# Performance work log

Measured on AMD Instinct MI355X. Metric: run time of the kernel, lower is better.

Reference implementation:

```python
import jax, jax.numpy as jnp
import numpy as np

B, INP, OUP, FGROUP, H, W = 32, 256, 256, 8, 64, 64
CG = INP // FGROUP  # channels per group in GLGF fc1 layers


def conv3x3(x, w):
    # x: (N,1,H,W), w: (1,1,3,3); stride 1, padding 1 (SAME)
    return jax.lax.conv_general_dilated(
        x, w, window_strides=(1, 1), padding='SAME',
        dimension_numbers=('NCHW', 'OIHW', 'NCHW'))


def setup_inputs() -> dict:
    key = jax.random.key(0)
    ks = jax.random.split(key, 8)
    return {
        'x': jax.random.normal(ks[0], (B, INP, H, W), dtype=jnp.float32),
        # GLGF params (all 1x1 convs, bias=False), stored as dense matrices
        'w1l': jax.random.normal(ks[1], (FGROUP, CG, CG), dtype=jnp.float32) * 0.05,   # wn_fc1_l (groups=fgroup)
        'w1g1': jax.random.normal(ks[2], (FGROUP, CG), dtype=jnp.float32) * 0.05,      # wn_fc1_g1 (inp->fgroup, groups=fgroup)
        'w1g2': jax.random.normal(ks[3], (INP, FGROUP), dtype=jnp.float32) * 0.05,     # wn_fc1_g2 (fgroup->inp dense)
        'w2l': jax.random.normal(ks[4], (INP, OUP), dtype=jnp.float32) * 0.05,         # wn_fc2_l (groups=inp): input ch i -> oup outputs
        'w2g': jax.random.normal(ks[5], (INP,), dtype=jnp.float32) * 0.05,             # wn_fc2_g (inp->1 dense)
        'conv1_w': jax.random.normal(ks[6], (1, 1, 3, 3), dtype=jnp.float32) * 0.1,
        'conv2_w': jax.random.normal(ks[7], (1, 1, 3, 3), dtype=jnp.float32) * 0.1,
    }


def reference(x, w1l, w1g1, w1g2, w2l, w2g, conv1_w, conv2_w):
    b, c, h, w_ = x.shape
    fgroup, cg, _ = w1l.shape
    oup = w2l.shape[1]

    # adaptive_avg_pool2d(x, (1,1)) -> (B, inp) descriptor
    g = x.mean(axis=(2, 3))                                   # (B, inp)
    gg = g.reshape(b, fgroup, cg)

    # GLGF: fc1_l (grouped) + fc1_g2(fc1_g1) (squeeze to fgroup then expand)
    local = jnp.einsum('bgi,goi->bgo', gg, w1l).reshape(b, c)  # (B, inp)
    glob = jnp.einsum('bgi,gi->bg', gg, w1g1) @ w1g2.T         # (B, inp)
    s = jax.nn.sigmoid(local + glob)                           # (B, inp)

    # fc2_l (groups=inp): torch channel order is (input_ch g, out j) -> g*oup + j
    # fc2_g adds a per-sample scalar to every channel
    xw = s[:, :, None] * w2l + (s @ w2g)[:, None, None]        # (B, inp, oup)
    # WA_1Conv reinterprets the flat (oup*inp) channels as (oup, inp)
    Wdyn = xw.reshape(b, oup, c)                               # (B, oup, inp)

    # grouped conv with groups=batch, ksize=1 == per-sample matmul
    y = jnp.einsum('bihw,boi->bohw', x, Wdyn)                  # (B, oup, H, W)

    # channel gating: mean over channels -> conv3x3 -> sigmoid -> conv3x3
    cmap = y.mean(axis=1, keepdims=True)                       # (B, 1, H, W)
    cmap = conv3x3(cmap, conv1_w)
    cmap = jax.nn.sigmoid(cmap)
    cmap = conv3x3(cmap, conv2_w)
    return y * cmap
```

## Files before the change

kernel.cpp:

```cpp
#include <hip/hip_runtime.h>
#include <hip/hip_bf16.h>

typedef float  f32x4  __attribute__((ext_vector_type(4)));
typedef short  bf16x8 __attribute__((ext_vector_type(8)));

__device__ __forceinline__ short f2bf(float f) {
    union { __hip_bfloat16 h; short s; } u;
    u.h = __float2bfloat16(f);
    return u.s;
}

__device__ __forceinline__ void gload_lds16(const void* g, void* l) {
    __builtin_amdgcn_global_load_lds(
        (const __attribute__((address_space(1))) unsigned int*)g,
        (__attribute__((address_space(3))) unsigned int*)l, 16, 0, 0);
}

__global__ __launch_bounds__(256) void transpose_kernel(const float* __restrict__ x,
                                                        short* __restrict__ xt,
                                                        float* __restrict__ gpart) {
    const int pchunk = blockIdx.x;
    const int c0 = blockIdx.y * 64;
    const int b  = blockIdx.z;
    const int tid = threadIdx.x;
    const int cpair = tid >> 3;
    const int poct  = tid & 7;
    const int p0 = pchunk * 64;

    __shared__ unsigned int tile[64 * 32];

    const float* rowA = x + ((size_t)(b * 256 + c0 + 2 * cpair)) * 4096 + p0 + poct * 8;
    const float* rowB = rowA + 4096;
    float av[8], bv[8];
    *reinterpret_cast<float4*>(&av[0]) = *reinterpret_cast<const float4*>(rowA);
    *reinterpret_cast<float4*>(&av[4]) = *reinterpret_cast<const float4*>(rowA + 4);
    *reinterpret_cast<float4*>(&bv[0]) = *reinterpret_cast<const float4*>(rowB);
    *reinterpret_cast<float4*>(&bv[4]) = *reinterpret_cast<const float4*>(rowB + 4);

    float sA = 0.f, sB = 0.f;
    #pragma unroll
    for (int e = 0; e < 8; ++e) { sA += av[e]; sB += bv[e]; }
    sA += __shfl_xor(sA, 1, 64); sA += __shfl_xor(sA, 2, 64); sA += __shfl_xor(sA, 4, 64);
    sB += __shfl_xor(sB, 1, 64); sB += __shfl_xor(sB, 2, 64); sB += __shfl_xor(sB, 4, 64);
    if (poct == 0) {
        gpart[((size_t)(b * 256 + c0 + 2 * cpair)) * 64 + pchunk] = sA;
        gpart[((size_t)(b * 256 + c0 + 2 * cpair + 1)) * 64 + pchunk] = sB;
    }

    const int s = cpair >> 2, w = cpair & 3;
    #pragma unroll
    for (int e = 0; e < 8; ++e) {
        int p = poct * 8 + e;
        unsigned int u = (unsigned int)(unsigned short)f2bf(av[e]) |
                         ((unsigned int)(unsigned short)f2bf(bv[e]) << 16);
        tile[p * 32 + ((s ^ poct) << 2) + w] = u;
    }
    __syncthreads();

    const int so = tid & 7;
    #pragma unroll
    for (int h = 0; h < 2; ++h) {
        int p = (tid >> 3) + h * 32;
        int sp = so ^ ((p >> 3) & 7);
        uint4 v = *reinterpret_cast<const uint4*>(&tile[p * 32 + sp * 4]);
        *reinterpret_cast<uint4*>(xt + ((size_t)b * 4096 + p0 + p) * 256 + c0 + so * 8) = v;
    }
}

__global__ __launch_bounds__(256) void prep_kernel(
    const float* __restrict__ gpart, const float* __restrict__ w1l,
    const float* __restrict__ w1g1, const float* __restrict__ w1g2,
    const float* __restrict__ w2l, const float* __restrict__ w2g,
    float* __restrict__ s_out, float* __restrict__ t_out,
    float* __restrict__ q_out, short* __restrict__ w2l_bf) {
    int b = blockIdx.x;
    int tid = threadIdx.x;
    if (b >= 32) {
        int seg = b - 32;
        const float* src = w2l + seg * 4096;
        short* dst = w2l_bf + seg * 4096;
        #pragma unroll
        for (int it = 0; it < 4; ++it) {
            float4 v = *reinterpret_cast<const float4*>(src + it * 1024 + tid * 4);
            short4 o;
            o.x = f2bf(v.x); o.y = f2bf(v.y); o.z = f2bf(v.z); o.w = f2bf(v.w);
            *reinterpret_cast<short4*>(dst + it * 1024 + tid * 4) = o;
        }
        return;
    }
    __shared__ float gs[256];
    __shared__ float zs[8];
    __shared__ float ss[256];
    __shared__ float red[4];
    {
        const float4* gp = reinterpret_cast<const float4*>(gpart + (size_t)(b * 256 + tid) * 64);
        float acc = 0.f;
        #pragma unroll
        for (int j = 0; j < 16; ++j) { float4 v = gp[j]; acc += v.x + v.y + v.z + v.w; }
        gs[tid] = acc * (1.0f / 4096.0f);
    }
    __syncthreads();
    if (tid < 8) {
        float z = 0.f;
        for (int i = 0; i < 32; ++i) z += gs[tid * 32 + i] * w1g1[tid * 32 + i];
        zs[tid] = z;
    }
    __syncthreads();
    int grp = tid >> 5, o = tid & 31;
    float local = 0.f;
    #pragma unroll 4
    for (int i = 0; i < 32; ++i) local += gs[grp * 32 + i] * w1l[grp * 1024 + o * 32 + i];
    float glob = 0.f;
    #pragma unroll
    for (int gg = 0; gg < 8; ++gg) glob += zs[gg] * w1g2[tid * 8 + gg];
    float sv = 1.0f / (1.0f + expf(-(local + glob)));
    ss[tid] = sv;
    s_out[b * 256 + tid] = sv;
    float tv = sv * w2g[tid];
    #pragma unroll
    for (int off = 32; off; off >>= 1) tv += __shfl_down(tv, off, 64);
    if ((tid & 63) == 0) red[tid >> 6] = tv;
    __syncthreads();
    float tb = red[0] + red[1] + red[2] + red[3];
    if (tid == 0) t_out[b] = tb;
    float v = 0.f;
    for (int o2 = 0; o2 < 256; ++o2) v += ss[o2] * w2l[o2 * 256 + tid];
    q_out[b * 256 + tid] = v * (1.0f / 256.0f) + tb;
}

__global__ __launch_bounds__(256) void cmap0_kernel(const float* __restrict__ x,
                                                    const float* __restrict__ q,
                                                    float* __restrict__ cmap0p,
                                                    float* __restrict__ xsump) {
    const int part = blockIdx.y;
    const int b = blockIdx.z;
    const int p = blockIdx.x * 1024 + threadIdx.x * 4;
    __shared__ float qs[64];
    if (threadIdx.x < 64) qs[threadIdx.x] = q[b * 256 + part * 64 + threadIdx.x];
    __syncthreads();
    const float* xb = x + ((size_t)(b * 256 + part * 64)) * 4096 + p;
    f32x4 a = {0.f, 0.f, 0.f, 0.f}, sm = {0.f, 0.f, 0.f, 0.f};
    #pragma unroll 8
    for (int i = 0; i < 64; ++i) {
        f32x4 v = *reinterpret_cast<const f32x4*>(xb + (size_t)i * 4096);
        a += qs[i] * v;
        sm += v;
    }
    *reinterpret_cast<f32x4*>(cmap0p + ((size_t)(part * 32 + b)) * 4096 + p) = a;
    *reinterpret_cast<f32x4*>(xsump  + ((size_t)(part * 32 + b)) * 4096 + p) = sm;
}

__global__ __launch_bounds__(256) void convs_kernel(const float* __restrict__ cmap0p,
                                                    const float* __restrict__ w9a,
                                                    const float* __restrict__ w9b,
                                                    float* __restrict__ out) {
    int b = blockIdx.x;
    int tid = threadIdx.x;
    __shared__ float img[4096];
    __shared__ float mid[4096];
    float wa[9], wb[9];
    #pragma unroll
    for (int i = 0; i < 9; ++i) { wa[i] = w9a[i]; wb[i] = w9b[i]; }
    {
        #pragma unroll
        for (int it = 0; it < 4; ++it) {
            int idx = it * 256 + tid;
            f32x4 v = {0.f, 0.f, 0.f, 0.f};
            #pragma unroll
            for (int part = 0; part < 4; ++part)
                v += *reinterpret_cast<const f32x4*>(cmap0p + ((size_t)(part * 32 + b)) * 4096 + idx * 4);
            *reinterpret_cast<f32x4*>(&img[idx * 4]) = v;
        }
    }
    __syncthreads();
    #pragma unroll
    for (int it = 0; it < 16; ++it) {
        int pix = it * 256 + tid;
        int y = pix >> 6, x0 = pix & 63;
        float acc = 0.f;
        #pragma unroll
        for (int dy = -1; dy <= 1; ++dy)
            #pragma unroll
            for (int dx = -1; dx <= 1; ++dx) {
                int yy = y + dy, xx = x0 + dx;
                if (yy >= 0 && yy < 64 && xx >= 0 && xx < 64)
                    acc += img[yy * 64 + xx] * wa[(dy + 1) * 3 + (dx + 1)];
            }
        mid[pix] = 1.0f / (1.0f + expf(-acc));
    }
    __syncthreads();
    #pragma unroll
    for (int it = 0; it < 16; ++it) {
        int pix = it * 256 + tid;
        int y = pix >> 6, x0 = pix & 63;
        float acc = 0.f;
        #pragma unroll
        for (int dy = -1; dy <= 1; ++dy)
            #pragma unroll
            for (int dx = -1; dx <= 1; ++dx) {
                int yy = y + dy, xx = x0 + dx;
                if (yy >= 0 && yy < 64 && xx >= 0 && xx < 64)
                    acc += mid[yy * 64 + xx] * wb[(dy + 1) * 3 + (dx + 1)];
            }
        out[(size_t)b * 4096 + pix] = acc;
    }
}

__global__ __launch_bounds__(512) void gemm_epi_kernel(
    const short* __restrict__ xt, const short* __restrict__ w2l_bf,
    const float* __restrict__ s, const float* __restrict__ t,
    const float* __restrict__ xsump, const float* __restrict__ cmap,
    float* __restrict__ out) {
    const int b  = blockIdx.z;
    const int p0 = blockIdx.x * 64;
    const int tid  = threadIdx.x;
    const int lane = tid & 63;
    const int w    = tid >> 6;
    const int wm = w >> 1, wn = w & 1;

    __shared__ short Alds[256 * 64];
    __shared__ short Xlds[64 * 64];

    const int sl   = (lane & 7) ^ (lane >> 3);
    const int lrow = lane >> 3;

    f32x4 acc[4][2] = {};

    for (int ks = 0; ks < 256; ks += 64) {
        #pragma unroll
        for (int j = 0; j < 4; ++j) {
            int chunk = w * 4 + j;
            int row = chunk * 8 + lrow;
            gload_lds16(w2l_bf + (size_t)row * 256 + ks + sl * 8,
                        (char*)Alds + chunk * 1024);
        }
        {
            int prow = w * 8 + lrow;
            gload_lds16(xt + ((size_t)b * 4096 + p0 + prow) * 256 + ks + sl * 8,
                        (char*)Xlds + w * 1024);
        }
        __syncthreads();
        #pragma unroll
        for (int kk = 0; kk < 2; ++kk) {
            bf16x8 af[4], bfr[2];
            const int ss = kk * 4 + (lane >> 4);
            #pragma unroll
            for (int m = 0; m < 4; ++m) {
                int o = wm * 64 + m * 16 + (lane & 15);
                af[m] = *reinterpret_cast<const bf16x8*>(
                    (char*)Alds + o * 128 + ((ss ^ (lane & 7)) * 16));
            }
            #pragma unroll
            for (int n = 0; n < 2; ++n) {
                int p = wn * 32 + n * 16 + (lane & 15);
                bfr[n] = *reinterpret_cast<const bf16x8*>(
                    (char*)Xlds + p * 128 + ((ss ^ (lane & 7)) * 16));
            }
            #pragma unroll
            for (int m = 0; m < 4; ++m)
                #pragma unroll
                for (int n = 0; n < 2; ++n)
                    acc[m][n] = __builtin_amdgcn_mfma_f32_16x16x32_bf16(af[m], bfr[n], acc[m][n], 0, 0, 0);
        }
        __syncthreads();
    }
    const float tb = t[b];
    #pragma unroll
    for (int n = 0; n < 2; ++n) {
        int p = p0 + wn * 32 + n * 16 + (lane & 15);
        float xs = 0.f;
        #pragma unroll
        for (int part = 0; part < 4; ++part)
            xs += xsump[((size_t)(part * 32 + b)) * 4096 + p];
        float cm = cmap[b * 4096 + p];
        float txs = tb * xs;
        #pragma unroll
        for (int m = 0; m < 4; ++m) {
            #pragma unroll
            for (int r = 0; r < 4; ++r) {
                int o = wm * 64 + m * 16 + (lane >> 4) * 4 + r;
                float yv = s[b * 256 + o] * acc[m][n][r] + txs;
                out[((size_t)b * 256 + o) * 4096 + p] = yv * cm;
            }
        }
    }
}

extern "C" void kernel_launch(void* const* d_in, const int* in_sizes, int n_in,
                              void* d_out, int out_size, void* d_ws, size_t ws_size,
                              hipStream_t stream) {
    const float* x       = (const float*)d_in[0];
    const float* w1l     = (const float*)d_in[1];
    const float* w1g1    = (const float*)d_in[2];
    const float* w1g2    = (const float*)d_in[3];
    const float* w2l     = (const float*)d_in[4];
    const float* w2g     = (const float*)d_in[5];
    const float* conv1_w = (const float*)d_in[6];
    const float* conv2_w = (const float*)d_in[7];
    float* out = (float*)d_out;

    float* wsf    = (float*)d_ws;
    float* s      = wsf;
    float* t      = wsf + 8192;
    float* q      = wsf + 8256;
    float* cmap0p = wsf + 16448;
    float* xsump  = wsf + 540736;
    float* cmap   = wsf + 1065024;
    float* gpart  = wsf + 1196096;
    short* w2l_bf = (short*)(wsf + 1720384);
    short* xt     = (short*)(wsf + 1753152);

    transpose_kernel<<<dim3(64, 4, 32), 256, 0, stream>>>(x, xt, gpart);
    prep_kernel<<<48, 256, 0, stream>>>(gpart, w1l, w1g1, w1g2, w2l, w2g, s, t, q, w2l_bf);
    cmap0_kernel<<<dim3(4, 4, 32), 256, 0, stream>>>(x, q, cmap0p, xsump);
    convs_kernel<<<32, 256, 0, stream>>>(cmap0p, conv1_w, conv2_w, cmap);
    gemm_epi_kernel<<<dim3(64, 1, 32), 512, 0, stream>>>(xt, w2l_bf, s, t, xsump, cmap, out);
}
```

Measured before the change: 142.0 us.

## Compute channel sums in transpose and read bf16 transposed x for cmap

The transpose kernel now also emits per-pixel channel partial sums, which removes the second full fp32 read of x in cmap0. cmap0 instead reads the bf16 channel-last copy with per-pixel dot products and writes a single cmap0 plus a t*xsum buffer. The 3x3 conv stage is split into row strips with halo recompute to raise block count, and the GEMM epilogue reads the precomputed t*xsum. The cost is more partial-sum traffic (16 parts), a bf16-precision cmap dot product, and redundant halo convolution.

```diff
diff --git a/kernel.cpp b/kernel.cpp
--- a/kernel.cpp
+++ b/kernel.cpp
@@ -18,9 +18,11 @@
 
 __global__ __launch_bounds__(256) void transpose_kernel(const float* __restrict__ x,
                                                         short* __restrict__ xt,
-                                                        float* __restrict__ gpart) {
+                                                        float* __restrict__ gpart,
+                                                        float* __restrict__ xsump) {
     const int pchunk = blockIdx.x;
-    const int c0 = blockIdx.y * 64;
+    const int cchunk = blockIdx.y;
+    const int c0 = cchunk * 64;
     const int b  = blockIdx.z;
     const int tid = threadIdx.x;
     const int cpair = tid >> 3;
@@ -47,6 +49,22 @@
         gpart[((size_t)(b * 256 + c0 + 2 * cpair + 1)) * 64 + pchunk] = sB;
     }
 
+    float xs[8];
+    #pragma unroll
+    for (int e = 0; e < 8; ++e) {
+        float v = av[e] + bv[e];
+        v += __shfl_xor(v, 8, 64);
+        v += __shfl_xor(v, 16, 64);
+        v += __shfl_xor(v, 32, 64);
+        xs[e] = v;
+    }
+    if ((tid & 56) == 0) {
+        int wv = tid >> 6;
+        float* dst = xsump + ((size_t)((cchunk * 4 + wv) * 32 + b)) * 4096 + p0 + poct * 8;
+        *reinterpret_cast<f32x4*>(dst)     = *reinterpret_cast<f32x4*>(&xs[0]);
+        *reinterpret_cast<f32x4*>(dst + 4) = *reinterpret_cast<f32x4*>(&xs[4]);
+    }
+
     const int s = cpair >> 2, w = cpair & 3;
     #pragma unroll
     for (int e = 0; e < 8; ++e) {
@@ -72,7 +90,7 @@
     const float* __restrict__ w1g1, const float* __restrict__ w1g2,
     const float* __restrict__ w2l, const float* __restrict__ w2g,
     float* __restrict__ s_out, float* __restrict__ t_out,
-    float* __restrict__ q_out, short* __restrict__ w2l_bf) {
+    float* __restrict__ vq_out, short* __restrict__ w2l_bf) {
     int b = blockIdx.x;
     int tid = threadIdx.x;
     if (b >= 32) {
@@ -125,92 +143,96 @@
     if (tid == 0) t_out[b] = tb;
     float v = 0.f;
     for (int o2 = 0; o2 < 256; ++o2) v += ss[o2] * w2l[o2 * 256 + tid];
-    q_out[b * 256 + tid] = v * (1.0f / 256.0f) + tb;
-}
-
-__global__ __launch_bounds__(256) void cmap0_kernel(const float* __restrict__ x,
-                                                    const float* __restrict__ q,
-                                                    float* __restrict__ cmap0p,
-                                                    float* __restrict__ xsump) {
-    const int part = blockIdx.y;
-    const int b = blockIdx.z;
-    const int p = blockIdx.x * 1024 + threadIdx.x * 4;
-    __shared__ float qs[64];
-    if (threadIdx.x < 64) qs[threadIdx.x] = q[b * 256 + part * 64 + threadIdx.x];
-    __syncthreads();
-    const float* xb = x + ((size_t)(b * 256 + part * 64)) * 4096 + p;
-    f32x4 a = {0.f, 0.f, 0.f, 0.f}, sm = {0.f, 0.f, 0.f, 0.f};
+    vq_out[b * 256 + tid] = v * (1.0f / 256.0f);
+}
+
+__global__ __launch_bounds__(256) void cmap0_kernel(const short* __restrict__ xt,
+                                                    const float* __restrict__ vq,
+                                                    const float* __restrict__ t,
+                                                    const float* __restrict__ xsump,
+                                                    float* __restrict__ cmap0,
+                                                    float* __restrict__ txs) {
+    const int b = blockIdx.y;
+    const int p = blockIdx.x * 256 + threadIdx.x;
+    __shared__ float vs[256];
+    vs[threadIdx.x] = vq[b * 256 + threadIdx.x];
+    __syncthreads();
+    const uint4* row = reinterpret_cast<const uint4*>(xt + ((size_t)b * 4096 + p) * 256);
+    float acc = 0.f;
     #pragma unroll 8
-    for (int i = 0; i < 64; ++i) {
-        f32x4 v = *reinterpret_cast<const f32x4*>(xb + (size_t)i * 4096);
-        a += qs[i] * v;
-        sm += v;
-    }
-    *reinterpret_cast<f32x4*>(cmap0p + ((size_t)(part * 32 + b)) * 4096 + p) = a;
-    *reinterpret_cast<f32x4*>(xsump  + ((size_t)(part * 32 + b)) * 4096 + p) = sm;
-}
-
-__global__ __launch_bounds__(256) void convs_kernel(const float* __restrict__ cmap0p,
+    for (int it = 0; it < 32; ++it) {
+        uint4 u = row[it];
+        const unsigned int* uw = reinterpret_cast<const unsigned int*>(&u);
+        #pragma unroll
+        for (int j = 0; j < 4; ++j) {
+            unsigned int wrd = uw[j];
+            union { unsigned int u; float f; } lo, hi;
+            lo.u = wrd << 16;
+            hi.u = wrd & 0xffff0000u;
+            acc += lo.f * vs[it * 8 + 2 * j] + hi.f * vs[it * 8 + 2 * j + 1];
+        }
+    }
+    float xs = 0.f;
+    #pragma unroll
+    for (int part = 0; part < 16; ++part)
+        xs += xsump[((size_t)(part * 32 + b)) * 4096 + p];
+    float tb = t[b];
+    float tx = tb * xs;
+    cmap0[b * 4096 + p] = acc + tx;
+    txs[b * 4096 + p] = tx;
+}
+
+__global__ __launch_bounds__(256) void convs_kernel(const float* __restrict__ cmap0,
                                                     const float* __restrict__ w9a,
                                                     const float* __restrict__ w9b,
-                                                    float* __restrict__ out) {
-    int b = blockIdx.x;
-    int tid = threadIdx.x;
-    __shared__ float img[4096];
-    __shared__ float mid[4096];
+                                                    float* __restrict__ cmap) {
+    const int strip = blockIdx.x;
+    const int b = blockIdx.y;
+    const int tid = threadIdx.x;
+    const int r0 = strip * 16;
+    const int rlo = (r0 == 0) ? 0 : r0 - 1;
+    const int rhi = (r0 + 16 > 63) ? 63 : r0 + 16;
+    const int cnt = rhi - rlo + 1;
+
+    __shared__ float mid[18 * 64];
     float wa[9], wb[9];
     #pragma unroll
     for (int i = 0; i < 9; ++i) { wa[i] = w9a[i]; wb[i] = w9b[i]; }
-    {
-        #pragma unroll
-        for (int it = 0; it < 4; ++it) {
-            int idx = it * 256 + tid;
-            f32x4 v = {0.f, 0.f, 0.f, 0.f};
-            #pragma unroll
-            for (int part = 0; part < 4; ++part)
-                v += *reinterpret_cast<const f32x4*>(cmap0p + ((size_t)(part * 32 + b)) * 4096 + idx * 4);
-            *reinterpret_cast<f32x4*>(&img[idx * 4]) = v;
-        }
-    }
-    __syncthreads();
-    #pragma unroll
-    for (int it = 0; it < 16; ++it) {
-        int pix = it * 256 + tid;
-        int y = pix >> 6, x0 = pix & 63;
+    const float* ib = cmap0 + (size_t)b * 4096;
+
+    for (int idx = tid; idx < cnt * 64; idx += 256) {
+        int r = rlo + (idx >> 6), cc = idx & 63;
         float acc = 0.f;
         #pragma unroll
         for (int dy = -1; dy <= 1; ++dy)
             #pragma unroll
             for (int dx = -1; dx <= 1; ++dx) {
-                int yy = y + dy, xx = x0 + dx;
-                if (yy >= 0 && yy < 64 && xx >= 0 && xx < 64)
-                    acc += img[yy * 64 + xx] * wa[(dy + 1) * 3 + (dx + 1)];
-            }
-        mid[pix] = 1.0f / (1.0f + expf(-acc));
-    }
-    __syncthreads();
-    #pragma unroll
-    for (int it = 0; it < 16; ++it) {
-        int pix = it * 256 + tid;
-        int y = pix >> 6, x0 = pix & 63;
+                int rr = r + dy, xx = cc + dx;
+                if (rr >= 0 && rr < 64 && xx >= 0 && xx < 64)
+                    acc += ib[rr * 64 + xx] * wa[(dy + 1) * 3 + (dx + 1)];
+            }
+        mid[idx] = 1.0f / (1.0f + expf(-acc));
+    }
+    __syncthreads();
+    for (int idx = tid; idx < 1024; idx += 256) {
+        int r = r0 + (idx >> 6), cc = idx & 63;
         float acc = 0.f;
         #pragma unroll
         for (int dy = -1; dy <= 1; ++dy)
             #pragma unroll
             for (int dx = -1; dx <= 1; ++dx) {
-                int yy = y + dy, xx = x0 + dx;
-                if (yy >= 0 && yy < 64 && xx >= 0 && xx < 64)
-                    acc += mid[yy * 64 + xx] * wb[(dy + 1) * 3 + (dx + 1)];
-            }
-        out[(size_t)b * 4096 + pix] = acc;
+                int rr = r + dy, xx = cc + dx;
+                if (rr >= 0 && rr < 64 && xx >= 0 && xx < 64)
+                    acc += mid[(rr - rlo) * 64 + xx] * wb[(dy + 1) * 3 + (dx + 1)];
+            }
+        cmap[(size_t)b * 4096 + r * 64 + cc] = acc;
     }
 }
 
 __global__ __launch_bounds__(512) void gemm_epi_kernel(
     const short* __restrict__ xt, const short* __restrict__ w2l_bf,
-    const float* __restrict__ s, const float* __restrict__ t,
-    const float* __restrict__ xsump, const float* __restrict__ cmap,
-    float* __restrict__ out) {
+    const float* __restrict__ s, const float* __restrict__ txs,
+    const float* __restrict__ cmap, float* __restrict__ out) {
     const int b  = blockIdx.z;
     const int p0 = blockIdx.x * 64;
     const int tid  = threadIdx.x;
@@ -264,22 +286,17 @@
         }
         __syncthreads();
     }
-    const float tb = t[b];
     #pragma unroll
     for (int n = 0; n < 2; ++n) {
         int p = p0 + wn * 32 + n * 16 + (lane & 15);
-        float xs = 0.f;
-        #pragma unroll
-        for (int part = 0; part < 4; ++part)
-            xs += xsump[((size_t)(part * 32 + b)) * 4096 + p];
+        float tx = txs[b * 4096 + p];
         float cm = cmap[b * 4096 + p];
-        float txs = tb * xs;
         #pragma unroll
         for (int m = 0; m < 4; ++m) {
             #pragma unroll
             for (int r = 0; r < 4; ++r) {
                 int o = wm * 64 + m * 16 + (lane >> 4) * 4 + r;
-                float yv = s[b * 256 + o] * acc[m][n][r] + txs;
+                float yv = s[b * 256 + o] * acc[m][n][r] + tx;
                 out[((size_t)b * 256 + o) * 4096 + p] = yv * cm;
             }
         }
@@ -302,17 +319,18 @@
     float* wsf    = (float*)d_ws;
     float* s      = wsf;
     float* t      = wsf + 8192;
-    float* q      = wsf + 8256;
-    float* cmap0p = wsf + 16448;
-    float* xsump  = wsf + 540736;
-    float* cmap   = wsf + 1065024;
-    float* gpart  = wsf + 1196096;
-    short* w2l_bf = (short*)(wsf + 1720384);
-    short* xt     = (short*)(wsf + 1753152);
-
-    transpose_kernel<<<dim3(64, 4, 32), 256, 0, stream>>>(x, xt, gpart);
-    prep_kernel<<<48, 256, 0, stream>>>(gpart, w1l, w1g1, w1g2, w2l, w2g, s, t, q, w2l_bf);
-    cmap0_kernel<<<dim3(4, 4, 32), 256, 0, stream>>>(x, q, cmap0p, xsump);
-    convs_kernel<<<32, 256, 0, stream>>>(cmap0p, conv1_w, conv2_w, cmap);
-    gemm_epi_kernel<<<dim3(64, 1, 32), 512, 0, stream>>>(xt, w2l_bf, s, t, xsump, cmap, out);
-}
+    float* vq     = wsf + 8256;
+    float* cmap0  = wsf + 16448;
+    float* txs    = wsf + 147520;
+    float* cmap   = wsf + 278592;
+    float* gpart  = wsf + 409664;
+    float* xsump  = wsf + 933952;
+    short* w2l_bf = (short*)(wsf + 3031104);
+    short* xt     = (short*)(wsf + 3063872);
+
+    transpose_kernel<<<dim3(64, 4, 32), 256, 0, stream>>>(x, xt, gpart, xsump);
+    prep_kernel<<<48, 256, 0, stream>>>(gpart, w1l, w1g1, w1g2, w2l, w2g, s, t, vq, w2l_bf);
+    cmap0_kernel<<<dim3(16, 32), 256, 0, stream>>>(xt, vq, t, xsump, cmap0, txs);
+    convs_kernel<<<dim3(4, 32), 256, 0, stream>>>(cmap0, conv1_w, conv2_w, cmap);
+    gemm_epi_kernel<<<dim3(64, 1, 32), 512, 0, stream>>>(xt, w2l_bf, s, txs, cmap, out);
+}
```

Result: faster. 129.6 us (-8.7%).
